# Performance work log

Hardware: AMD Instinct MI355X
Metric: run time of the kernel (lower is better)

## Reference

```python
import jax, jax.numpy as jnp
import numpy as np

WINDOW_SIZE = 2
CART_PIXEL_WIDTH = 640
CART_RESOLUTION = 0.2592
# even width -> (w/2 - 0.5) * res
CART_MIN_RANGE = (CART_PIXEL_WIDTH / 2 - 0.5) * CART_RESOLUTION


def setup_inputs() -> dict:
    key = jax.random.key(0)
    k1, k2, k3 = jax.random.split(key, 3)
    B, W, N = 64, WINDOW_SIZE, 100000
    keypoint_coords = jax.random.uniform(k1, (B * W, N, 2), dtype=jnp.float32) * CART_PIXEL_WIDTH
    tgt_coords = jax.random.uniform(k2, (B, N, 2), dtype=jnp.float32) * CART_PIXEL_WIDTH
    weights = jax.random.uniform(k3, (B, 1, N), dtype=jnp.float32) + 1e-3
    return {"keypoint_coords": keypoint_coords, "tgt_coords": tgt_coords, "weights": weights}


def _convert_to_radar_frame(p):
    # p: [B, N, 2] pixel coords -> radar-frame metric coords
    # R = [[0, -res], [res, 0]]; t = [cmin, -cmin]
    x = -CART_RESOLUTION * p[..., 1] + CART_MIN_RANGE
    y = CART_RESOLUTION * p[..., 0] - CART_MIN_RANGE
    return jnp.stack([x, y], axis=-1)  # [B, N, 2]


def _svd_forward(keypoint_coords, tgt_coords, weights):
    src = keypoint_coords[::WINDOW_SIZE]                # [B, N, 2]
    src = _convert_to_radar_frame(src)
    tgt = _convert_to_radar_frame(tgt_coords)
    # pad 2D -> 3D with zeros, then transpose to [B, 3, N]
    src = jnp.pad(src, ((0, 0), (0, 0), (0, 1))).transpose(0, 2, 1)
    tgt = jnp.pad(tgt, ((0, 0), (0, 0), (0, 1))).transpose(0, 2, 1)

    w = jnp.sum(weights, axis=2, keepdims=True)         # [B, 1, 1]
    src_centroid = jnp.sum(src * weights, axis=2, keepdims=True) / w  # [B, 3, 1]
    tgt_centroid = jnp.sum(tgt * weights, axis=2, keepdims=True) / w
    src_c = src - src_centroid
    tgt_c = tgt - tgt_centroid
    # weighted cross-covariance: [B, 3, 3]
    Wc = jnp.einsum('bin,bjn->bij', tgt_c * weights, src_c) / w

    U, _, Vh = jnp.linalg.svd(Wc)                       # square -> full == reduced
    det_UV = jnp.linalg.det(U) * jnp.linalg.det(Vh)     # det(V) == det(Vh) for 3x3? no: det(Vh)=det(V^T)=det(V)
    # R = U @ diag(1, 1, det) @ V^T ; scale last column of U by det
    s = jnp.stack([jnp.ones_like(det_UV), jnp.ones_like(det_UV), det_UV], axis=-1)  # [B, 3]
    R_tgt_src = jnp.einsum('bik,bk,bkj->bij', U, s, Vh)

    t_tgt_src_insrc = src_centroid - jnp.einsum('bki,bkj->bij', R_tgt_src, tgt_centroid)
    t_src_tgt_intgt = -jnp.einsum('bik,bkj->bij', R_tgt_src, t_tgt_src_insrc)
    return R_tgt_src.transpose(0, 2, 1), t_src_tgt_intgt


def reference(keypoint_coords, tgt_coords, weights):
    return _svd_forward(keypoint_coords, tgt_coords, weights)
```

## Files before the change

### kernel.cpp

```cpp
#include <hip/hip_runtime.h>

#define RES  0.2592
#define MINR 82.8144

__global__ __launch_bounds__(256) void svd_reduce(
    const float4* __restrict__ kp,
    const float4* __restrict__ tg,
    const float2* __restrict__ wt,
    double* __restrict__ ws,
    int npairs, int bpb)
{
    const int batch = blockIdx.y;
    const float4* __restrict__ src = kp + (size_t)(2 * batch) * npairs;
    const float4* __restrict__ tgt = tg + (size_t)batch * npairs;
    const float2* __restrict__ wp  = wt + (size_t)batch * npairs;

    double aW = 0, aSx = 0, aSy = 0, aTx = 0, aTy = 0;
    double aXX = 0, aXY = 0, aYX = 0, aYY = 0;

    for (int i = blockIdx.x * 256 + threadIdx.x; i < npairs; i += bpb * 256) {
        float4 s4 = src[i];
        float4 t4 = tgt[i];
        float2 w2 = wp[i];

        {
            double w  = (double)w2.x;
            double sx = MINR - RES * (double)s4.y;
            double sy = RES * (double)s4.x - MINR;
            double tx = MINR - RES * (double)t4.y;
            double ty = RES * (double)t4.x - MINR;
            double wtx = w * tx, wty = w * ty;
            aW  += w;
            aSx += w * sx;   aSy += w * sy;
            aTx += wtx;      aTy += wty;
            aXX += wtx * sx; aXY += wtx * sy;
            aYX += wty * sx; aYY += wty * sy;
        }
        {
            double w  = (double)w2.y;
            double sx = MINR - RES * (double)s4.w;
            double sy = RES * (double)s4.z - MINR;
            double tx = MINR - RES * (double)t4.w;
            double ty = RES * (double)t4.z - MINR;
            double wtx = w * tx, wty = w * ty;
            aW  += w;
            aSx += w * sx;   aSy += w * sy;
            aTx += wtx;      aTy += wty;
            aXX += wtx * sx; aXY += wtx * sy;
            aYX += wty * sx; aYY += wty * sy;
        }
    }

    double acc[9] = {aW, aSx, aSy, aTx, aTy, aXX, aXY, aYX, aYY};

    #pragma unroll
    for (int k = 0; k < 9; k++) {
        #pragma unroll
        for (int off = 32; off > 0; off >>= 1)
            acc[k] += __shfl_down(acc[k], off, 64);
    }

    __shared__ double sred[4][9];
    const int lane = threadIdx.x & 63;
    const int wid  = threadIdx.x >> 6;
    if (lane == 0) {
        #pragma unroll
        for (int k = 0; k < 9; k++) sred[wid][k] = acc[k];
    }
    __syncthreads();
    if (threadIdx.x < 9) {
        double v = sred[0][threadIdx.x] + sred[1][threadIdx.x] +
                   sred[2][threadIdx.x] + sred[3][threadIdx.x];
        unsafeAtomicAdd(&ws[(size_t)batch * 9 + threadIdx.x], v);
    }
}

__global__ void svd_finalize(const double* __restrict__ ws,
                             float* __restrict__ out, int B)
{
    int b = blockIdx.x * blockDim.x + threadIdx.x;
    if (b >= B) return;
    const double* s = ws + (size_t)b * 9;
    double W  = s[0];
    double Sx = s[1], Sy = s[2], Tx = s[3], Ty = s[4];
    double Mxx = s[5], Mxy = s[6], Myx = s[7], Myy = s[8];

    double invW = 1.0 / W;
    double a  = (Mxx - Tx * Sx * invW) * invW;
    double bb = (Mxy - Tx * Sy * invW) * invW;
    double c  = (Myx - Ty * Sx * invW) * invW;
    double d  = (Myy - Ty * Sy * invW) * invW;

    double h1 = sqrt((a + d) * (a + d) + (bb - c) * (bb - c));
    double h2 = sqrt((a - d) * (a - d) + (bb + c) * (bb + c));

    double q00, q01, q10, q11, sgn;
    if (h1 >= h2) {
        double inv = 1.0 / h1;
        q00 = (a + d) * inv;  q01 = (bb - c) * inv;
        q10 = (c - bb) * inv; q11 = (a + d) * inv;
        sgn = 1.0;
    } else {
        double inv = 1.0 / h2;
        q00 = (a - d) * inv;  q01 = (bb + c) * inv;
        q10 = (bb + c) * inv; q11 = (d - a) * inv;
        sgn = -1.0;
    }

    double sx = Sx * invW, sy = Sy * invW;
    double tx = Tx * invW, ty = Ty * invW;

    double t1x = sx - (q00 * tx + q10 * ty);
    double t1y = sy - (q01 * tx + q11 * ty);
    double ox = -(q00 * t1x + q01 * t1y);
    double oy = -(q10 * t1x + q11 * t1y);

    float* R = out + (size_t)b * 9;
    R[0] = (float)q00; R[1] = (float)q10; R[2] = 0.0f;
    R[3] = (float)q01; R[4] = (float)q11; R[5] = 0.0f;
    R[6] = 0.0f;       R[7] = 0.0f;       R[8] = (float)sgn;

    float* T = out + (size_t)B * 9 + (size_t)b * 3;
    T[0] = (float)ox; T[1] = (float)oy; T[2] = 0.0f;
}

extern "C" void kernel_launch(void* const* d_in, const int* in_sizes, int n_in,
                              void* d_out, int out_size, void* d_ws, size_t ws_size,
                              hipStream_t stream) {
    const float* kp = (const float*)d_in[0];
    const float* tg = (const float*)d_in[1];
    const float* wt = (const float*)d_in[2];
    float* out = (float*)d_out;

    const int B = out_size / 12;
    const int N = in_sizes[2] / B;
    const int npairs = N / 2;
    const int BPB = 32;

    hipMemsetAsync(d_ws, 0, (size_t)B * 9 * sizeof(double), stream);

    dim3 grid(BPB, B);
    svd_reduce<<<grid, 256, 0, stream>>>(
        (const float4*)kp, (const float4*)tg, (const float2*)wt,
        (double*)d_ws, npairs, BPB);

    svd_finalize<<<(B + 63) / 64, 64, 0, stream>>>((const double*)d_ws, out, B);
}
```

Before: 194.5 us.

## Accumulate raw pixel moments, widen loads, replace atomics with per-block partials

Accumulates the weighted moments on raw pixel coordinates and applies the radar-frame affine transform algebraically in the finalize kernel, which removes per-point FP64 multiply-adds. Each thread now processes four points per iteration using float4 weight loads. Per-block partial sums are written to the workspace instead of being combined with atomics, which also removes the memset launch; finalize then sums the 32 partials per batch. The catch is that the moments are now taken about uncentered raw coordinates, and the expanded formulas are only correct if every sign in them is right.

```diff
diff --git a/kernel.cpp b/kernel.cpp
--- a/kernel.cpp
+++ b/kernel.cpp
@@ -6,52 +6,51 @@
 __global__ __launch_bounds__(256) void svd_reduce(
     const float4* __restrict__ kp,
     const float4* __restrict__ tg,
-    const float2* __restrict__ wt,
+    const float4* __restrict__ wq4,
+    const float2* __restrict__ wt2,
     double* __restrict__ ws,
     int npairs, int bpb)
 {
-    const int batch = blockIdx.y;
-    const float4* __restrict__ src = kp + (size_t)(2 * batch) * npairs;
-    const float4* __restrict__ tgt = tg + (size_t)batch * npairs;
-    const float2* __restrict__ wp  = wt + (size_t)batch * npairs;
+    const int batch  = blockIdx.y;
+    const int nquads = npairs >> 1;
+    const float4* __restrict__ src = kp  + (size_t)(2 * batch) * npairs;
+    const float4* __restrict__ tgt = tg  + (size_t)batch * npairs;
+    const float4* __restrict__ wq  = wq4 + (size_t)batch * nquads;
 
-    double aW = 0, aSx = 0, aSy = 0, aTx = 0, aTy = 0;
+    double aW = 0, aPx = 0, aPy = 0, aQx = 0, aQy = 0;
     double aXX = 0, aXY = 0, aYX = 0, aYY = 0;
 
-    for (int i = blockIdx.x * 256 + threadIdx.x; i < npairs; i += bpb * 256) {
-        float4 s4 = src[i];
-        float4 t4 = tgt[i];
-        float2 w2 = wp[i];
+    #define POINT(wf, sxf, syf, txf, tyf) do {                 \
+        double w  = (double)(wf);                              \
+        double sx = (double)(sxf), sy = (double)(syf);         \
+        double tx = (double)(txf), ty = (double)(tyf);         \
+        double wtx = w * tx, wty = w * ty;                     \
+        aW  += w;                                              \
+        aPx += w * sx;   aPy += w * sy;                        \
+        aQx += wtx;      aQy += wty;                           \
+        aXX += wtx * sx; aXY += wtx * sy;                      \
+        aYX += wty * sx; aYY += wty * sy;                      \
+    } while (0)
 
-        {
-            double w  = (double)w2.x;
-            double sx = MINR - RES * (double)s4.y;
-            double sy = RES * (double)s4.x - MINR;
-            double tx = MINR - RES * (double)t4.y;
-            double ty = RES * (double)t4.x - MINR;
-            double wtx = w * tx, wty = w * ty;
-            aW  += w;
-            aSx += w * sx;   aSy += w * sy;
-            aTx += wtx;      aTy += wty;
-            aXX += wtx * sx; aXY += wtx * sy;
-            aYX += wty * sx; aYY += wty * sy;
-        }
-        {
-            double w  = (double)w2.y;
-            double sx = MINR - RES * (double)s4.w;
-            double sy = RES * (double)s4.z - MINR;
-            double tx = MINR - RES * (double)t4.w;
-            double ty = RES * (double)t4.z - MINR;
-            double wtx = w * tx, wty = w * ty;
-            aW  += w;
-            aSx += w * sx;   aSy += w * sy;
-            aTx += wtx;      aTy += wty;
-            aXX += wtx * sx; aXY += wtx * sy;
-            aYX += wty * sx; aYY += wty * sy;
-        }
+    for (int i = blockIdx.x * 256 + threadIdx.x; i < nquads; i += bpb * 256) {
+        float4 s0 = src[2 * i], s1 = src[2 * i + 1];
+        float4 t0 = tgt[2 * i], t1 = tgt[2 * i + 1];
+        float4 w4 = wq[i];
+        POINT(w4.x, s0.x, s0.y, t0.x, t0.y);
+        POINT(w4.y, s0.z, s0.w, t0.z, t0.w);
+        POINT(w4.z, s1.x, s1.y, t1.x, t1.y);
+        POINT(w4.w, s1.z, s1.w, t1.z, t1.w);
     }
+    if ((npairs & 1) && blockIdx.x == 0 && threadIdx.x == 0) {
+        int i = npairs - 1;
+        float4 s4 = src[i], t4 = tgt[i];
+        float2 w2 = wt2[(size_t)batch * npairs + i];
+        POINT(w2.x, s4.x, s4.y, t4.x, t4.y);
+        POINT(w2.y, s4.z, s4.w, t4.z, t4.w);
+    }
+    #undef POINT
 
-    double acc[9] = {aW, aSx, aSy, aTx, aTy, aXX, aXY, aYX, aYY};
+    double acc[9] = {aW, aPx, aPy, aQx, aQy, aXX, aXY, aYX, aYY};
 
     #pragma unroll
     for (int k = 0; k < 9; k++) {
@@ -71,19 +70,37 @@
     if (threadIdx.x < 9) {
         double v = sred[0][threadIdx.x] + sred[1][threadIdx.x] +
                    sred[2][threadIdx.x] + sred[3][threadIdx.x];
-        unsafeAtomicAdd(&ws[(size_t)batch * 9 + threadIdx.x], v);
+        ws[((size_t)batch * bpb + blockIdx.x) * 9 + threadIdx.x] = v;
     }
 }
 
 __global__ void svd_finalize(const double* __restrict__ ws,
-                             float* __restrict__ out, int B)
+                             float* __restrict__ out, int B, int bpb)
 {
     int b = blockIdx.x * blockDim.x + threadIdx.x;
     if (b >= B) return;
-    const double* s = ws + (size_t)b * 9;
-    double W  = s[0];
-    double Sx = s[1], Sy = s[2], Tx = s[3], Ty = s[4];
-    double Mxx = s[5], Mxy = s[6], Myx = s[7], Myy = s[8];
+
+    double m[9] = {0, 0, 0, 0, 0, 0, 0, 0, 0};
+    const double* p = ws + (size_t)b * bpb * 9;
+    for (int j = 0; j < bpb; ++j) {
+        #pragma unroll
+        for (int k = 0; k < 9; ++k) m[k] += p[j * 9 + k];
+    }
+
+    double W  = m[0];
+    double Px = m[1], Py = m[2], Qx = m[3], Qy = m[4];
+    double Rxx = m[5], Rxy = m[6], Ryx = m[7], Ryy = m[8];
+
+    const double MR = MINR * RES, RR = RES * RES;
+    double MW = MINR * W;
+    double Sx = MW - RES * Py;
+    double Sy = RES * Px - MW;
+    double Tx = MW - RES * Qy;
+    double Ty = RES * Qx - MW;
+    double Mxx = MINR * MW - MR * (Py + Qy) + RR * Ryy;
+    double Mxy = MR * Px - MINR * MW + MR * Qy - RR * Ryx;
+    double Myx = MR * Qx + MR * Py - MINR * MW - RR * Rxy;
+    double Myy = RR * Rxx - MR * (Px + Qx) + MINR * MW;
 
     double invW = 1.0 / W;
     double a  = (Mxx - Tx * Sx * invW) * invW;
@@ -137,12 +154,11 @@
     const int npairs = N / 2;
     const int BPB = 32;
 
-    hipMemsetAsync(d_ws, 0, (size_t)B * 9 * sizeof(double), stream);
-
     dim3 grid(BPB, B);
     svd_reduce<<<grid, 256, 0, stream>>>(
-        (const float4*)kp, (const float4*)tg, (const float2*)wt,
+        (const float4*)kp, (const float4*)tg,
+        (const float4*)wt, (const float2*)wt,
         (double*)d_ws, npairs, BPB);
 
-    svd_finalize<<<(B + 63) / 64, 64, 0, stream>>>((const double*)d_ws, out, B);
+    svd_finalize<<<(B + 63) / 64, 64, 0, stream>>>((const double*)d_ws, out, B, BPB);
 }
```

New measurement: 208.8 us. +7.3%, slower.
